# Performance work log

Measured on AMD Instinct MI355X. Metric: run time of the kernel, lower is better.

The kernel has to match this reference:

```python
import jax, jax.numpy as jnp
import numpy as np

SCALE = 4.0  # VeRA scale hyperparameter


def setup_inputs() -> dict:
    key = jax.random.key(0)
    ks = jax.random.split(key, 7)
    T, IN, OUT, R = 8192, 4096, 4096, 256
    return {
        "x": jax.random.normal(ks[0], (T, IN), dtype=jnp.float32),
        "base_weight": jax.random.normal(ks[1], (OUT, IN), dtype=jnp.float32) * 0.02,
        "base_bias": jax.random.normal(ks[2], (OUT,), dtype=jnp.float32) * 0.02,
        "vera_random_A": jax.random.normal(ks[3], (R, IN), dtype=jnp.float32) * (1.0 / np.sqrt(IN)),
        "vera_random_B": jax.random.normal(ks[4], (OUT, R), dtype=jnp.float32) * (1.0 / np.sqrt(R)),
        "vera_d": jax.random.normal(ks[5], (R,), dtype=jnp.float32) * 0.01,
        "vera_b": 0.1 * jnp.ones((OUT,), dtype=jnp.float32),
    }


def reference(x, base_weight, base_bias, vera_random_A, vera_random_B, vera_d, vera_b):
    # delta_W = scale * diag(vera_b) @ B @ diag(vera_d) @ A  -> row/col scaling, no diag matmuls
    # shapes: B (out, r), A (r, in), delta (out, in)
    delta = SCALE * jnp.einsum("or,ri->oi", vera_b[:, None] * vera_random_B, vera_d[:, None] * vera_random_A)
    # linear: y = x @ (W + delta)^T + bias
    return x @ (base_weight + delta).T + base_bias
```

## Files before the change

kernel.cpp:

```cpp
#include <hip/hip_runtime.h>


typedef __attribute__((ext_vector_type(8))) short short8;
typedef __attribute__((ext_vector_type(4))) float f32x4;

__device__ __forceinline__ unsigned short f2bf(float f) {
  union { float f; unsigned int u; } c; c.f = f;
  unsigned int u = c.u;
  unsigned int r = (u + 0x7fffu + ((u >> 16) & 1u)) >> 16;
  return (unsigned short)r;
}

__device__ __forceinline__ void gl2lds16(const unsigned short* g, unsigned short* l) {
  __builtin_amdgcn_global_load_lds(
      (const __attribute__((address_space(1))) unsigned int*)g,
      (__attribute__((address_space(3))) unsigned int*)l, 16, 0, 0);
}

__global__ __launch_bounds__(256) void k_pre(const float* __restrict__ x,
                                             unsigned short* __restrict__ xb,
                                             const float* __restrict__ Bv,
                                             const float* __restrict__ Av,
                                             const float* __restrict__ dv,
                                             const float* __restrict__ bv,
                                             unsigned short* __restrict__ Bd,
                                             unsigned short* __restrict__ AbT) {
  __shared__ float tl[32][33];
  const int blk = blockIdx.x;
  const int tid = threadIdx.x;
  if (blk < 32768) {
    int i = blk * 256 + tid;
    const float4 v = ((const float4*)x)[i];
    union { unsigned short u[4]; unsigned long long ll; } o;
    o.u[0] = f2bf(v.x); o.u[1] = f2bf(v.y); o.u[2] = f2bf(v.z); o.u[3] = f2bf(v.w);
    ((unsigned long long*)xb)[i] = o.ll;
  } else if (blk < 36864) {
    int idx = (blk - 32768) * 256 + tid;
    int o = idx >> 8, r = idx & 255;
    Bd[idx] = f2bf(4.0f * bv[o] * Bv[idx] * dv[r]);
  } else {
    int blk2 = blk - 36864;
    int ti = blk2 >> 3;
    int tr = blk2 & 7;
#pragma unroll
    for (int s = 0; s < 4; ++s) {
      int r = tr * 32 + s * 8 + (tid >> 5);
      int i = ti * 32 + (tid & 31);
      tl[s * 8 + (tid >> 5)][tid & 31] = Av[(size_t)r * 4096 + i];
    }
    __syncthreads();
#pragma unroll
    for (int s = 0; s < 4; ++s) {
      int iloc = s * 8 + (tid >> 5);
      int rloc = tid & 31;
      AbT[(size_t)(ti * 32 + iloc) * 256 + tr * 32 + rloc] = f2bf(tl[rloc][iloc]);
    }
  }
}

template <int FOLD>
__global__ __launch_bounds__(256) void gemm_bt(const unsigned short* __restrict__ Amat,
                                               const unsigned short* __restrict__ Bmat,
                                               int K, int N,
                                               const float* __restrict__ extra,
                                               float* __restrict__ outF,
                                               unsigned short* __restrict__ outB) {
  __shared__ unsigned short As[128 * 32];
  __shared__ unsigned short Bs[128 * 32];

  const int tid  = threadIdx.x;
  const int lane = tid & 63;
  const int wave = tid >> 6;
  const int wm   = wave >> 1;
  const int wn   = wave & 1;
  const int quad = lane >> 4;
  const int m16  = lane & 15;

  const int blockN = blockIdx.x * 128;
  const int blockM = blockIdx.y * 128;

  const int ldRow  = lane >> 2;
  const int dstCol = (lane & 3) * 8;
  const int srcCol = ((lane & 3) ^ ((lane >> 4) & 3)) * 8;
  const int seg0   = wave * 2;

  const size_t aOff0 = (size_t)(blockM + seg0 * 16 + ldRow) * K + srcCol;
  const size_t aOff1 = (size_t)(blockM + seg0 * 16 + 16 + ldRow) * K + srcCol;
  const size_t bOff0 = (size_t)(blockN + seg0 * 16 + ldRow) * K + srcCol;
  const size_t bOff1 = (size_t)(blockN + seg0 * 16 + 16 + ldRow) * K + srcCol;

  unsigned short* lA0 = &As[(seg0 * 16 + ldRow) * 32 + dstCol];
  unsigned short* lA1 = &As[(seg0 * 16 + 16 + ldRow) * 32 + dstCol];
  unsigned short* lB0 = &Bs[(seg0 * 16 + ldRow) * 32 + dstCol];
  unsigned short* lB1 = &Bs[(seg0 * 16 + 16 + ldRow) * 32 + dstCol];

  f32x4 acc[4][4];
#pragma unroll
  for (int i = 0; i < 4; ++i)
#pragma unroll
    for (int j = 0; j < 4; ++j) acc[i][j] = (f32x4){0.f, 0.f, 0.f, 0.f};

  const short8* Asv = (const short8*)As;
  const short8* Bsv = (const short8*)Bs;
  const int qsw = quad ^ ((m16 >> 2) & 3);

  for (int k0 = 0; k0 < K; k0 += 32) {
    __syncthreads();
    gl2lds16(Amat + aOff0 + k0, lA0);
    gl2lds16(Amat + aOff1 + k0, lA1);
    gl2lds16(Bmat + bOff0 + k0, lB0);
    gl2lds16(Bmat + bOff1 + k0, lB1);
    __syncthreads();

    short8 af[4], bf[4];
#pragma unroll
    for (int t = 0; t < 4; ++t) {
      af[t] = Asv[(wm * 64 + t * 16 + m16) * 4 + qsw];
      bf[t] = Bsv[(wn * 64 + t * 16 + m16) * 4 + qsw];
    }
#pragma unroll
    for (int mt = 0; mt < 4; ++mt)
#pragma unroll
      for (int nt = 0; nt < 4; ++nt)
        acc[mt][nt] = __builtin_amdgcn_mfma_f32_16x16x32_bf16(af[mt], bf[nt], acc[mt][nt], 0, 0, 0);
  }

#pragma unroll
  for (int mt = 0; mt < 4; ++mt) {
    const int row0 = blockM + wm * 64 + mt * 16 + quad * 4;
#pragma unroll
    for (int nt = 0; nt < 4; ++nt) {
      const int col = blockN + wn * 64 + nt * 16 + m16;
      f32x4 v = acc[mt][nt];
      if (FOLD) {
#pragma unroll
        for (int r = 0; r < 4; ++r) {
          size_t o = (size_t)(row0 + r) * N + col;
          outB[o] = f2bf(extra[o] + v[r]);
        }
      } else {
        const float bv = extra[col];
#pragma unroll
        for (int r = 0; r < 4; ++r) {
          size_t o = (size_t)(row0 + r) * N + col;
          outF[o] = v[r] + bv;
        }
      }
    }
  }
}

extern "C" void kernel_launch(void* const* d_in, const int* in_sizes, int n_in,
                              void* d_out, int out_size, void* d_ws, size_t ws_size,
                              hipStream_t stream) {
  const float* x    = (const float*)d_in[0];
  const float* W    = (const float*)d_in[1];
  const float* bias = (const float*)d_in[2];
  const float* A    = (const float*)d_in[3];
  const float* B    = (const float*)d_in[4];
  const float* dv   = (const float*)d_in[5];
  const float* bv   = (const float*)d_in[6];
  float* out = (float*)d_out;

  char* ws = (char*)d_ws;
  unsigned short* xb  = (unsigned short*)ws;
  unsigned short* Wc  = (unsigned short*)(ws + (size_t)(64 << 20));
  unsigned short* Bd  = (unsigned short*)(ws + (size_t)(96 << 20));
  unsigned short* AbT = (unsigned short*)(ws + (size_t)(98 << 20));

  hipLaunchKernelGGL(k_pre, dim3(37888), dim3(256), 0, stream,
                     x, xb, B, A, dv, bv, Bd, AbT);
  hipLaunchKernelGGL((gemm_bt<1>), dim3(32, 32), dim3(256), 0, stream,
                     Bd, AbT, 256, 4096, W, (float*)nullptr, Wc);
  hipLaunchKernelGGL((gemm_bt<0>), dim3(32, 64), dim3(256), 0, stream,
                     xb, Wc, 4096, 4096, bias, out, (unsigned short*)nullptr);
}
```

Before: 640.1 us.

## Double GEMM K-tile to 64 with 8-way LDS swizzle and batch cast blocks

The GEMM kernels now stage a 64-wide K slice per iteration instead of 32, which halves the number of barrier pairs per K and issues eight global-to-LDS loads per thread. The LDS layout uses an 8-chunk XOR swizzle to match the wider rows. The prep kernel's x-to-bf16 cast now handles four float4 per thread, cutting block count. The cost is doubled LDS per block, which may lower occupancy, and there is still no double buffering.

Result: faster. 587.8 us (-8.2%).

```diff
diff --git a/kernel.cpp b/kernel.cpp
--- a/kernel.cpp
+++ b/kernel.cpp
@@ -28,18 +28,21 @@
   __shared__ float tl[32][33];
   const int blk = blockIdx.x;
   const int tid = threadIdx.x;
-  if (blk < 32768) {
-    int i = blk * 256 + tid;
-    const float4 v = ((const float4*)x)[i];
-    union { unsigned short u[4]; unsigned long long ll; } o;
-    o.u[0] = f2bf(v.x); o.u[1] = f2bf(v.y); o.u[2] = f2bf(v.z); o.u[3] = f2bf(v.w);
-    ((unsigned long long*)xb)[i] = o.ll;
-  } else if (blk < 36864) {
-    int idx = (blk - 32768) * 256 + tid;
+  if (blk < 8192) {
+#pragma unroll
+    for (int s = 0; s < 4; ++s) {
+      int i = blk * 1024 + s * 256 + tid;
+      const float4 v = ((const float4*)x)[i];
+      union { unsigned short u[4]; unsigned long long ll; } o;
+      o.u[0] = f2bf(v.x); o.u[1] = f2bf(v.y); o.u[2] = f2bf(v.z); o.u[3] = f2bf(v.w);
+      ((unsigned long long*)xb)[i] = o.ll;
+    }
+  } else if (blk < 12288) {
+    int idx = (blk - 8192) * 256 + tid;
     int o = idx >> 8, r = idx & 255;
     Bd[idx] = f2bf(4.0f * bv[o] * Bv[idx] * dv[r]);
   } else {
-    int blk2 = blk - 36864;
+    int blk2 = blk - 12288;
     int ti = blk2 >> 3;
     int tr = blk2 & 7;
 #pragma unroll
@@ -65,8 +68,8 @@
                                                const float* __restrict__ extra,
                                                float* __restrict__ outF,
                                                unsigned short* __restrict__ outB) {
-  __shared__ unsigned short As[128 * 32];
-  __shared__ unsigned short Bs[128 * 32];
+  __shared__ unsigned short As[128 * 64];
+  __shared__ unsigned short Bs[128 * 64];
 
   const int tid  = threadIdx.x;
   const int lane = tid & 63;
@@ -75,24 +78,25 @@
   const int wn   = wave & 1;
   const int quad = lane >> 4;
   const int m16  = lane & 15;
+  const int s7   = m16 & 7;
 
   const int blockN = blockIdx.x * 128;
   const int blockM = blockIdx.y * 128;
 
-  const int ldRow  = lane >> 2;
-  const int dstCol = (lane & 3) * 8;
-  const int srcCol = ((lane & 3) ^ ((lane >> 4) & 3)) * 8;
-  const int seg0   = wave * 2;
+  const int c    = tid & 7;
+  const int rsub = tid >> 3;
 
-  const size_t aOff0 = (size_t)(blockM + seg0 * 16 + ldRow) * K + srcCol;
-  const size_t aOff1 = (size_t)(blockM + seg0 * 16 + 16 + ldRow) * K + srcCol;
-  const size_t bOff0 = (size_t)(blockN + seg0 * 16 + ldRow) * K + srcCol;
-  const size_t bOff1 = (size_t)(blockN + seg0 * 16 + 16 + ldRow) * K + srcCol;
-
-  unsigned short* lA0 = &As[(seg0 * 16 + ldRow) * 32 + dstCol];
-  unsigned short* lA1 = &As[(seg0 * 16 + 16 + ldRow) * 32 + dstCol];
-  unsigned short* lB0 = &Bs[(seg0 * 16 + ldRow) * 32 + dstCol];
-  unsigned short* lB1 = &Bs[(seg0 * 16 + 16 + ldRow) * 32 + dstCol];
+  size_t aOff[4], bOff[4];
+  unsigned short *dA[4], *dB[4];
+#pragma unroll
+  for (int n = 0; n < 4; ++n) {
+    const int r = n * 32 + rsub;
+    const int src = (c ^ (r & 7)) * 8;
+    aOff[n] = (size_t)(blockM + r) * K + src;
+    bOff[n] = (size_t)(blockN + r) * K + src;
+    dA[n] = &As[(size_t)n * 2048 + tid * 8];
+    dB[n] = &Bs[(size_t)n * 2048 + tid * 8];
+  }
 
   f32x4 acc[4][4];
 #pragma unroll
@@ -102,27 +106,31 @@
 
   const short8* Asv = (const short8*)As;
   const short8* Bsv = (const short8*)Bs;
-  const int qsw = quad ^ ((m16 >> 2) & 3);
 
-  for (int k0 = 0; k0 < K; k0 += 32) {
+  for (int k0 = 0; k0 < K; k0 += 64) {
     __syncthreads();
-    gl2lds16(Amat + aOff0 + k0, lA0);
-    gl2lds16(Amat + aOff1 + k0, lA1);
-    gl2lds16(Bmat + bOff0 + k0, lB0);
-    gl2lds16(Bmat + bOff1 + k0, lB1);
+#pragma unroll
+    for (int n = 0; n < 4; ++n) {
+      gl2lds16(Amat + aOff[n] + k0, dA[n]);
+      gl2lds16(Bmat + bOff[n] + k0, dB[n]);
+    }
     __syncthreads();
 
-    short8 af[4], bf[4];
 #pragma unroll
-    for (int t = 0; t < 4; ++t) {
-      af[t] = Asv[(wm * 64 + t * 16 + m16) * 4 + qsw];
-      bf[t] = Bsv[(wn * 64 + t * 16 + m16) * 4 + qsw];
+    for (int h = 0; h < 2; ++h) {
+      const int qs = (h * 4 + quad) ^ s7;
+      short8 af[4], bf[4];
+#pragma unroll
+      for (int t = 0; t < 4; ++t) {
+        af[t] = Asv[(wm * 64 + t * 16 + m16) * 8 + qs];
+        bf[t] = Bsv[(wn * 64 + t * 16 + m16) * 8 + qs];
+      }
+#pragma unroll
+      for (int mt = 0; mt < 4; ++mt)
+#pragma unroll
+        for (int nt = 0; nt < 4; ++nt)
+          acc[mt][nt] = __builtin_amdgcn_mfma_f32_16x16x32_bf16(af[mt], bf[nt], acc[mt][nt], 0, 0, 0);
     }
-#pragma unroll
-    for (int mt = 0; mt < 4; ++mt)
-#pragma unroll
-      for (int nt = 0; nt < 4; ++nt)
-        acc[mt][nt] = __builtin_amdgcn_mfma_f32_16x16x32_bf16(af[mt], bf[nt], acc[mt][nt], 0, 0, 0);
   }
 
 #pragma unroll
@@ -168,7 +176,7 @@
   unsigned short* Bd  = (unsigned short*)(ws + (size_t)(96 << 20));
   unsigned short* AbT = (unsigned short*)(ws + (size_t)(98 << 20));
 
-  hipLaunchKernelGGL(k_pre, dim3(37888), dim3(256), 0, stream,
+  hipLaunchKernelGGL(k_pre, dim3(13312), dim3(256), 0, stream,
                      x, xb, B, A, dv, bv, Bd, AbT);
   hipLaunchKernelGGL((gemm_bt<1>), dim3(32, 32), dim3(256), 0, stream,
                      Bd, AbT, 256, 4096, W, (float*)nullptr, Wc);
```
